# Performance work log

Hardware: AMD Instinct MI355X
Metric: run time of the kernel (lower is better)

The kernel has to match this reference:

```python
import jax, jax.numpy as jnp
import numpy as np

SIZE_IMG = 512
STRIDE = 32
N_ANCHOR = 9
BOUND_AC_LO, BOUND_AC_HI = -0.2, 1.2
EPS = 1e-05
IOU_SCALE = 10000
NEG_TH_ACGT = int(IOU_SCALE * 0.3)
POS_TH_ACGT = int(IOU_SCALE * 0.5)
POS_TH_GTAC = int(IOU_SCALE * 0.01)
NUM_POS_RPN = 128
NUM_NEG_RPN = 128
B, N_GT = 512, 32


def _anchors_rel(size_img, stride):
    h_fm = w_fm = size_img // stride
    # scales: closest floor power of 2 of min image side
    smax = 2 ** (size_img).bit_length()
    scales = np.array([smax >> 3, smax >> 2, smax >> 1], dtype=np.float32)
    sqrt2 = 1.4142135624
    ratio_hw = np.array([[sqrt2, sqrt2 / 2], [1, 1], [sqrt2 / 2, sqrt2]], dtype=np.float32)
    # (9,2) heights/widths: 3 scales x 3 ratios
    hw = (scales[:, None, None] * ratio_hw[None]).reshape(9, 2)
    ys = (np.arange(h_fm, dtype=np.float32) * stride + stride // 2)
    xs = (np.arange(w_fm, dtype=np.float32) * stride + stride // 2)
    cy = np.tile(ys[:, None, None], (1, w_fm, N_ANCHOR))
    cx = np.tile(xs[None, :, None], (h_fm, 1, N_ANCHOR))
    ctr = np.stack([cy, cx], axis=-1)                      # (H,W,9,2)
    hw_half = 0.5 * np.tile(hw[None, None], (h_fm, w_fm, 1, 1))
    ac_abs = np.concatenate([ctr - hw_half, ctr + hw_half], axis=-1).reshape(-1, 4)
    ac = ac_abs / np.float32(size_img)                     # relative (ymin,xmin,ymax,xmax)
    keep = ((ac[:, 0] >= BOUND_AC_LO) & (ac[:, 1] >= BOUND_AC_LO)
            & (ac[:, 2] <= BOUND_AC_HI) & (ac[:, 3] <= BOUND_AC_HI)
            & (ac[:, 2] > ac[:, 0]) & (ac[:, 3] > ac[:, 1]))
    return ac[keep].astype(np.float32)                     # (1384, 4)


def setup_inputs() -> dict:
    key = jax.random.key(0)
    k1, k2, k3, k4 = jax.random.split(key, 4)
    # valid GT boxes: sorted coord pairs in [0,1]
    yy = jnp.sort(jax.random.uniform(k1, (B, N_GT, 2)), axis=-1)
    xx = jnp.sort(jax.random.uniform(k2, (B, N_GT, 2)), axis=-1)
    bx_gt = jnp.stack([yy[..., 0], xx[..., 0], yy[..., 1], xx[..., 1]], axis=-1)
    ac_val = jnp.asarray(_anchors_rel(SIZE_IMG, STRIDE))
    rand_pos = jax.random.uniform(k3, (B, ac_val.shape[0]))
    rand_neg = jax.random.uniform(k4, (B, ac_val.shape[0]))
    return {"bx_gt": bx_gt, "ac_val": ac_val, "rand_pos": rand_pos, "rand_neg": rand_neg}


def _iou_mat(ac, gt):
    # ac (N_ac,4), gt (B,N_gt,4) -> (B,N_ac,N_gt)
    a = ac[None, :, None, :]
    g = gt[:, None, :, :]
    ih = jnp.clip(jnp.minimum(a[..., 2], g[..., 2]) - jnp.maximum(a[..., 0], g[..., 0]), 0.0)
    iw = jnp.clip(jnp.minimum(a[..., 3], g[..., 3]) - jnp.maximum(a[..., 1], g[..., 1]), 0.0)
    inter = ih * iw
    area_ac = (ac[:, 2] - ac[:, 0]) * (ac[:, 3] - ac[:, 1])
    area_gt = (gt[..., 2] - gt[..., 0]) * (gt[..., 3] - gt[..., 1])
    union = area_ac[None, :, None] + area_gt[:, None, :] - inter
    return inter / (union + EPS)


def _bbox2delta(bx_l, bx_r):
    h_r = jnp.maximum(bx_r[..., 2] - bx_r[..., 0], EPS)
    w_r = jnp.maximum(bx_r[..., 3] - bx_r[..., 1], EPS)
    yc_r = bx_r[..., 0] + 0.5 * (bx_r[..., 2] - bx_r[..., 0])
    xc_r = bx_r[..., 1] + 0.5 * (bx_r[..., 3] - bx_r[..., 1])
    h_l = bx_l[..., 2] - bx_l[..., 0]
    w_l = bx_l[..., 3] - bx_l[..., 1]
    yc_l = bx_l[..., 0] + 0.5 * h_l
    xc_l = bx_l[..., 1] + 0.5 * w_l
    d = jnp.stack([(xc_l - xc_r) / w_r, (yc_l - yc_r) / h_r,
                   jnp.log(w_l / w_r), jnp.log(h_l / h_r)], axis=-1)
    return jnp.clip(d, -10.0, 10.0)


def _sample_mask(mask, num, rand):
    th = num / (jnp.sum(mask, axis=-1, keepdims=True) + 1e-06)
    return jnp.where(rand < th, 1.0, 0.0) * mask


def reference(bx_gt, ac_val, rand_pos, rand_neg):
    iou = _iou_mat(ac_val, bx_gt)                          # (B, N_ac, N_gt)
    ious = (iou * IOU_SCALE).astype(jnp.int32)             # scale-integer IoU
    best_gt = jnp.argmax(ious, axis=-1)                    # (B, N_ac)
    iou_acgt = jnp.max(ious, axis=-1)                      # (B, N_ac)
    best_ac = jnp.argmax(ious, axis=1)                     # (B, N_gt)
    iou_gtac = jnp.max(ious, axis=1)                       # (B, N_gt)
    b, n_ac = iou_acgt.shape
    valid_gtac = (iou_gtac >= POS_TH_GTAC).astype(jnp.float32)
    pos_gtac = jnp.zeros((b, n_ac), jnp.float32).at[
        jnp.arange(b)[:, None], best_ac].max(valid_gtac) > 0.5
    pos = (iou_acgt >= POS_TH_ACGT) | pos_gtac             # (B, N_ac)
    neg = (iou_acgt < NEG_TH_ACGT) & (~pos)
    gt_match = bx_gt[jnp.arange(b)[:, None], best_gt]      # (B, N_ac, 4)
    bx_tgt = jnp.where(pos[..., None], gt_match,
                       jnp.where(neg[..., None], -2.0, -1.0))
    coor_sum = jnp.sum(bx_tgt, axis=-1)
    mask_fg = jnp.where(coor_sum > -4.0, 1.0, 0.0)
    mask_bg = jnp.where(coor_sum <= -8.0, 1.0, 0.0)
    mask_pos = _sample_mask(mask_fg, NUM_POS_RPN, rand_pos)
    mask_neg = _sample_mask(mask_bg, NUM_NEG_RPN, rand_neg)
    ac_b = jnp.broadcast_to(ac_val[None], bx_tgt.shape)
    bx_safe = jnp.where(pos[..., None], bx_tgt, ac_b)      # avoid log of negatives
    bx_del = _bbox2delta(bx_safe, ac_b)
    return jnp.concatenate(
        [bx_tgt, bx_del, mask_pos[..., None], mask_neg[..., None]], axis=-1)
```

## Files before the change

kernel.cpp:

```cpp
#include <hip/hip_runtime.h>

#define NGT   32
#define EPSF  1e-5f
#define GTAC_BIT (1 << 20)
#define APT   3
#define K1SPAN (APT * 256)

__global__ __launch_bounds__(256) void rpn_k1(
    const float* __restrict__ bx_gt,
    const float* __restrict__ ac_val,
    int* __restrict__ pack,
    int* __restrict__ colkey,
    int* __restrict__ partial,
    int n_ac)
{
    #pragma clang fp contract(off)
    const int b = blockIdx.y, chunk = blockIdx.x, tid = threadIdx.x;
    const int w = tid >> 6, lane = tid & 63;

    __shared__ int s_wk[NGT * 4];
    __shared__ int s_c[8];

    const float4* __restrict__ gtp = (const float4*)(bx_gt + (size_t)b * NGT * 4);

    int ckey[NGT];
    #pragma unroll
    for (int g = 0; g < NGT; ++g) ckey[g] = 0;

    int cf = 0, cb = 0;

    for (int j = 0; j < APT; ++j) {
        const int a = chunk * K1SPAN + j * 256 + tid;
        const bool active = (a < n_ac);
        float a0 = 0.f, a1 = 0.f, a2 = 0.f, a3 = 0.f;
        if (active) {
            float4 av = ((const float4*)ac_val)[a];
            a0 = av.x; a1 = av.y; a2 = av.z; a3 = av.w;
        }
        const float area = (a2 - a0) * (a3 - a1);

        int rkey = -1;
        const int akey = active ? (4095 - a) : -1;
        #pragma unroll
        for (int g = 0; g < NGT; ++g) {
            const float4 g4 = gtp[g];
            const float area_g = (g4.z - g4.x) * (g4.w - g4.y);
            float ih = fmaxf(fminf(a2, g4.z) - fmaxf(a0, g4.x), 0.0f);
            float iw = fmaxf(fminf(a3, g4.w) - fmaxf(a1, g4.y), 0.0f);
            float inter = ih * iw;
            float uni = area + area_g - inter;
            float iou = inter / (uni + EPSF);
            int v = (int)(iou * 10000.0f);
            int rk = (v << 5) | (31 - g);
            rkey = max(rkey, rk);
            int key = active ? ((v << 12) | (4095 - a)) : 0;
            ckey[g] = max(ckey[g], key);
        }
        if (active) {
            pack[(size_t)b * n_ac + a] = rkey;
            const int vmax = rkey >> 5;
            cf += (vmax >= 5000);
            cb += (vmax < 3000);
        }
    }

    #pragma unroll
    for (int g = 0; g < NGT; ++g) {
        int k = ckey[g];
        #pragma unroll
        for (int off = 32; off >= 1; off >>= 1)
            k = max(k, __shfl_xor(k, off, 64));
        if (lane == 0) s_wk[g*4 + w] = k;
    }

    #pragma unroll
    for (int off = 32; off >= 1; off >>= 1) {
        cf += __shfl_xor(cf, off, 64);
        cb += __shfl_xor(cb, off, 64);
    }
    if (lane == 0) { s_c[w*2] = cf; s_c[w*2+1] = cb; }
    __syncthreads();

    if (tid < NGT) {
        int k = max(max(s_wk[tid*4+0], s_wk[tid*4+1]),
                    max(s_wk[tid*4+2], s_wk[tid*4+3]));
        atomicMax(&colkey[b * NGT + tid], k);
    }
    if (tid == 0) {
        partial[(b * gridDim.x + chunk) * 2 + 0] = s_c[0] + s_c[2] + s_c[4] + s_c[6];
        partial[(b * gridDim.x + chunk) * 2 + 1] = s_c[1] + s_c[3] + s_c[5] + s_c[7];
    }
}

__global__ __launch_bounds__(64) void rpn_k2(
    int* __restrict__ pack,
    const int* __restrict__ colkey,
    const int* __restrict__ partial,
    float* __restrict__ th,
    int n_ac, int n_chunk)
{
    const int b = blockIdx.x, tid = threadIdx.x;

    int pf = 0, pb = 0;
    if (tid < n_chunk) {
        pf = partial[(b * n_chunk + tid) * 2 + 0];
        pb = partial[(b * n_chunk + tid) * 2 + 1];
    }
    #pragma unroll
    for (int off = 32; off >= 1; off >>= 1) {
        pf += __shfl_xor(pf, off, 64);
        pb += __shfl_xor(pb, off, 64);
    }

    int valid = 0, a = 0;
    if (tid < NGT) {
        int key = colkey[b * NGT + tid];
        int v = key >> 12;
        a = 4095 - (key & 4095);
        valid = (v >= 100);
    }
    int av = valid ? a : (0x10000 + tid);
    bool dup = false;
    for (int gp = 0; gp < NGT; ++gp) {
        int o = __shfl(av, gp, 64);
        if (gp < tid && o == av) dup = true;
    }
    bool contrib = valid && !dup;
    int rm = 0x7FFF;
    if (contrib) rm = pack[(size_t)b * n_ac + a] >> 5;
    unsigned long long m1 = __ballot(contrib && rm < 5000);
    unsigned long long m2 = __ballot(contrib && rm < 3000);

    if (contrib) atomicOr(&pack[(size_t)b * n_ac + a], GTAC_BIT);

    if (tid == 0) {
        int cf = pf + __popcll(m1);
        int cb = pb - __popcll(m2);
        th[b*2 + 0] = 128.0f / ((float)cf + 1e-6f);
        th[b*2 + 1] = 128.0f / ((float)cb + 1e-6f);
    }
}

__global__ __launch_bounds__(256) void rpn_k3(
    const float* __restrict__ bx_gt,
    const float* __restrict__ ac_val,
    const float* __restrict__ rand_pos,
    const float* __restrict__ rand_neg,
    const int* __restrict__ pack,
    const float* __restrict__ th,
    float* __restrict__ out,
    int n_ac)
{
    #pragma clang fp contract(off)
    const int b = blockIdx.y, chunk = blockIdx.x, tid = threadIdx.x;

    __shared__ float s_gt[NGT * 4];
    __shared__ float s_o[10 * 257];

    if (tid < NGT * 4) s_gt[tid] = bx_gt[(size_t)b * NGT * 4 + tid];
    __syncthreads();

    const int a = chunk * 256 + tid;
    if (a < n_ac) {
        const float th_pos = th[b*2 + 0];
        const float th_neg = th[b*2 + 1];
        const int p = pack[(size_t)b * n_ac + a];
        const bool gtac = (p & GTAC_BIT) != 0;
        const int rm = (p >> 5) & 0x7FFF;
        const int bg = 31 - (p & 31);
        const bool pos = (rm >= 5000) || gtac;
        const bool neg = !pos && (rm < 3000);

        const float4 avv = ((const float4*)ac_val)[a];
        const float a0 = avv.x, a1 = avv.y, a2 = avv.z, a3 = avv.w;

        float o0, o1, o2, o3, o4, o5, o6, o7;
        if (pos) {
            float g0 = s_gt[bg*4+0], g1 = s_gt[bg*4+1];
            float g2 = s_gt[bg*4+2], g3 = s_gt[bg*4+3];
            o0 = g0; o1 = g1; o2 = g2; o3 = g3;
            float hr = fmaxf(a2 - a0, EPSF);
            float wr = fmaxf(a3 - a1, EPSF);
            float ycr = a0 + 0.5f * (a2 - a0);
            float xcr = a1 + 0.5f * (a3 - a1);
            float hl = g2 - g0, wl = g3 - g1;
            float ycl = g0 + 0.5f * hl;
            float xcl = g1 + 0.5f * wl;
            o4 = fminf(fmaxf((xcl - xcr) / wr, -10.0f), 10.0f);
            o5 = fminf(fmaxf((ycl - ycr) / hr, -10.0f), 10.0f);
            o6 = fminf(fmaxf(logf(wl / wr), -10.0f), 10.0f);
            o7 = fminf(fmaxf(logf(hl / hr), -10.0f), 10.0f);
        } else {
            float t = neg ? -2.0f : -1.0f;
            o0 = o1 = o2 = o3 = t;
            o4 = o5 = o6 = o7 = 0.0f;
        }
        const float o8 = (pos && rand_pos[(size_t)b * n_ac + a] < th_pos) ? 1.0f : 0.0f;
        const float o9 = (neg && rand_neg[(size_t)b * n_ac + a] < th_neg) ? 1.0f : 0.0f;

        s_o[0*257 + tid] = o0; s_o[1*257 + tid] = o1;
        s_o[2*257 + tid] = o2; s_o[3*257 + tid] = o3;
        s_o[4*257 + tid] = o4; s_o[5*257 + tid] = o5;
        s_o[6*257 + tid] = o6; s_o[7*257 + tid] = o7;
        s_o[8*257 + tid] = o8; s_o[9*257 + tid] = o9;
    }
    __syncthreads();

    const int na_blk = min(256, n_ac - chunk * 256);
    const int nd = na_blk * 10;
    float* dst = out + ((size_t)b * n_ac + (size_t)chunk * 256) * 10;
    #pragma unroll
    for (int m = 0; m < 10; ++m) {
        const int idx = m * 256 + tid;
        if (idx < nd) {
            const int al = idx / 10, k = idx - al * 10;
            dst[idx] = s_o[k * 257 + al];
        }
    }
}

extern "C" void kernel_launch(void* const* d_in, const int* in_sizes, int n_in,
                              void* d_out, int out_size, void* d_ws, size_t ws_size,
                              hipStream_t stream) {
    const float* bx_gt    = (const float*)d_in[0];
    const float* ac_val   = (const float*)d_in[1];
    const float* rand_pos = (const float*)d_in[2];
    const float* rand_neg = (const float*)d_in[3];
    float* out = (float*)d_out;

    const int n_ac     = in_sizes[1] / 4;
    const int B        = in_sizes[2] / n_ac;
    const int n_chunk1 = (n_ac + K1SPAN - 1) / K1SPAN;
    const int n_chunk3 = (n_ac + 255) / 256;

    int* pack    = (int*)d_ws;
    int* colkey  = pack + (size_t)B * n_ac;
    int* partial = colkey + (size_t)B * NGT;
    float* th    = (float*)(partial + (size_t)B * n_chunk1 * 2);

    rpn_k1<<<dim3(n_chunk1, B), 256, 0, stream>>>(bx_gt, ac_val, pack, colkey, partial, n_ac);
    rpn_k2<<<B, 64, 0, stream>>>(pack, colkey, partial, th, n_ac, n_chunk1);
    rpn_k3<<<dim3(n_chunk3, B), 256, 0, stream>>>(bx_gt, ac_val, rand_pos, rand_neg,
                                                  pack, th, out, n_ac);
}
```

Baseline: 114.3 us.

## Fuse three RPN kernels into one per-batch block with shared-memory state

Merges the IoU/argmax kernel, the GT-to-anchor fixup kernel and the output kernel into a single kernel with one 256-thread block per image. The per-anchor pack array, column keys, counts and thresholds stay in LDS instead of global workspace. This removes two kernel launches, the global atomics and the workspace round-trips. In exchange the grid drops to B blocks, each looping over all anchors serially, so there is less parallelism per image. It also adds a MAXA limit of 2048 anchors.

```diff
diff --git a/kernel.cpp b/kernel.cpp
--- a/kernel.cpp
+++ b/kernel.cpp
@@ -1,46 +1,43 @@
 #include <hip/hip_runtime.h>
 
 #define NGT   32
+#define MAXA  2048
 #define EPSF  1e-5f
 #define GTAC_BIT (1 << 20)
-#define APT   3
-#define K1SPAN (APT * 256)
 
-__global__ __launch_bounds__(256) void rpn_k1(
+__global__ __launch_bounds__(256) void rpn_fused(
     const float* __restrict__ bx_gt,
     const float* __restrict__ ac_val,
-    int* __restrict__ pack,
-    int* __restrict__ colkey,
-    int* __restrict__ partial,
+    const float* __restrict__ rand_pos,
+    const float* __restrict__ rand_neg,
+    float* __restrict__ out,
     int n_ac)
 {
     #pragma clang fp contract(off)
-    const int b = blockIdx.y, chunk = blockIdx.x, tid = threadIdx.x;
+    const int b = blockIdx.x, tid = threadIdx.x;
     const int w = tid >> 6, lane = tid & 63;
 
-    __shared__ int s_wk[NGT * 4];
-    __shared__ int s_c[8];
+    __shared__ int   s_pack[MAXA];
+    __shared__ int   s_wk[NGT * 4];
+    __shared__ int   s_c[8];
+    __shared__ float s_th[2];
+    __shared__ float s_gt[NGT * 4];
+    __shared__ float s_o[10 * 257];
+
+    if (tid < NGT * 4) s_gt[tid] = bx_gt[(size_t)b * NGT * 4 + tid];
 
     const float4* __restrict__ gtp = (const float4*)(bx_gt + (size_t)b * NGT * 4);
 
     int ckey[NGT];
     #pragma unroll
     for (int g = 0; g < NGT; ++g) ckey[g] = 0;
-
     int cf = 0, cb = 0;
 
-    for (int j = 0; j < APT; ++j) {
-        const int a = chunk * K1SPAN + j * 256 + tid;
-        const bool active = (a < n_ac);
-        float a0 = 0.f, a1 = 0.f, a2 = 0.f, a3 = 0.f;
-        if (active) {
-            float4 av = ((const float4*)ac_val)[a];
-            a0 = av.x; a1 = av.y; a2 = av.z; a3 = av.w;
-        }
+    for (int a = tid; a < n_ac; a += 256) {
+        const float4 av = ((const float4*)ac_val)[a];
+        const float a0 = av.x, a1 = av.y, a2 = av.z, a3 = av.w;
         const float area = (a2 - a0) * (a3 - a1);
-
         int rkey = -1;
-        const int akey = active ? (4095 - a) : -1;
         #pragma unroll
         for (int g = 0; g < NGT; ++g) {
             const float4 g4 = gtp[g];
@@ -51,17 +48,13 @@
             float uni = area + area_g - inter;
             float iou = inter / (uni + EPSF);
             int v = (int)(iou * 10000.0f);
-            int rk = (v << 5) | (31 - g);
-            rkey = max(rkey, rk);
-            int key = active ? ((v << 12) | (4095 - a)) : 0;
-            ckey[g] = max(ckey[g], key);
+            rkey = max(rkey, (v << 5) | (31 - g));
+            ckey[g] = max(ckey[g], (v << 12) | (4095 - a));
         }
-        if (active) {
-            pack[(size_t)b * n_ac + a] = rkey;
-            const int vmax = rkey >> 5;
-            cf += (vmax >= 5000);
-            cb += (vmax < 3000);
-        }
+        s_pack[a] = rkey;
+        const int vmax = rkey >> 5;
+        cf += (vmax >= 5000);
+        cb += (vmax < 3000);
     }
 
     #pragma unroll
@@ -72,7 +65,6 @@
             k = max(k, __shfl_xor(k, off, 64));
         if (lane == 0) s_wk[g*4 + w] = k;
     }
-
     #pragma unroll
     for (int off = 32; off >= 1; off >>= 1) {
         cf += __shfl_xor(cf, off, 64);
@@ -81,141 +73,96 @@
     if (lane == 0) { s_c[w*2] = cf; s_c[w*2+1] = cb; }
     __syncthreads();
 
-    if (tid < NGT) {
-        int k = max(max(s_wk[tid*4+0], s_wk[tid*4+1]),
-                    max(s_wk[tid*4+2], s_wk[tid*4+3]));
-        atomicMax(&colkey[b * NGT + tid], k);
-    }
-    if (tid == 0) {
-        partial[(b * gridDim.x + chunk) * 2 + 0] = s_c[0] + s_c[2] + s_c[4] + s_c[6];
-        partial[(b * gridDim.x + chunk) * 2 + 1] = s_c[1] + s_c[3] + s_c[5] + s_c[7];
-    }
-}
-
-__global__ __launch_bounds__(64) void rpn_k2(
-    int* __restrict__ pack,
-    const int* __restrict__ colkey,
-    const int* __restrict__ partial,
-    float* __restrict__ th,
-    int n_ac, int n_chunk)
-{
-    const int b = blockIdx.x, tid = threadIdx.x;
-
-    int pf = 0, pb = 0;
-    if (tid < n_chunk) {
-        pf = partial[(b * n_chunk + tid) * 2 + 0];
-        pb = partial[(b * n_chunk + tid) * 2 + 1];
-    }
-    #pragma unroll
-    for (int off = 32; off >= 1; off >>= 1) {
-        pf += __shfl_xor(pf, off, 64);
-        pb += __shfl_xor(pb, off, 64);
-    }
-
-    int valid = 0, a = 0;
-    if (tid < NGT) {
-        int key = colkey[b * NGT + tid];
-        int v = key >> 12;
-        a = 4095 - (key & 4095);
-        valid = (v >= 100);
-    }
-    int av = valid ? a : (0x10000 + tid);
-    bool dup = false;
-    for (int gp = 0; gp < NGT; ++gp) {
-        int o = __shfl(av, gp, 64);
-        if (gp < tid && o == av) dup = true;
-    }
-    bool contrib = valid && !dup;
-    int rm = 0x7FFF;
-    if (contrib) rm = pack[(size_t)b * n_ac + a] >> 5;
-    unsigned long long m1 = __ballot(contrib && rm < 5000);
-    unsigned long long m2 = __ballot(contrib && rm < 3000);
-
-    if (contrib) atomicOr(&pack[(size_t)b * n_ac + a], GTAC_BIT);
-
-    if (tid == 0) {
-        int cf = pf + __popcll(m1);
-        int cb = pb - __popcll(m2);
-        th[b*2 + 0] = 128.0f / ((float)cf + 1e-6f);
-        th[b*2 + 1] = 128.0f / ((float)cb + 1e-6f);
-    }
-}
-
-__global__ __launch_bounds__(256) void rpn_k3(
-    const float* __restrict__ bx_gt,
-    const float* __restrict__ ac_val,
-    const float* __restrict__ rand_pos,
-    const float* __restrict__ rand_neg,
-    const int* __restrict__ pack,
-    const float* __restrict__ th,
-    float* __restrict__ out,
-    int n_ac)
-{
-    #pragma clang fp contract(off)
-    const int b = blockIdx.y, chunk = blockIdx.x, tid = threadIdx.x;
-
-    __shared__ float s_gt[NGT * 4];
-    __shared__ float s_o[10 * 257];
-
-    if (tid < NGT * 4) s_gt[tid] = bx_gt[(size_t)b * NGT * 4 + tid];
-    __syncthreads();
-
-    const int a = chunk * 256 + tid;
-    if (a < n_ac) {
-        const float th_pos = th[b*2 + 0];
-        const float th_neg = th[b*2 + 1];
-        const int p = pack[(size_t)b * n_ac + a];
-        const bool gtac = (p & GTAC_BIT) != 0;
-        const int rm = (p >> 5) & 0x7FFF;
-        const int bg = 31 - (p & 31);
-        const bool pos = (rm >= 5000) || gtac;
-        const bool neg = !pos && (rm < 3000);
-
-        const float4 avv = ((const float4*)ac_val)[a];
-        const float a0 = avv.x, a1 = avv.y, a2 = avv.z, a3 = avv.w;
-
-        float o0, o1, o2, o3, o4, o5, o6, o7;
-        if (pos) {
-            float g0 = s_gt[bg*4+0], g1 = s_gt[bg*4+1];
-            float g2 = s_gt[bg*4+2], g3 = s_gt[bg*4+3];
-            o0 = g0; o1 = g1; o2 = g2; o3 = g3;
-            float hr = fmaxf(a2 - a0, EPSF);
-            float wr = fmaxf(a3 - a1, EPSF);
-            float ycr = a0 + 0.5f * (a2 - a0);
-            float xcr = a1 + 0.5f * (a3 - a1);
-            float hl = g2 - g0, wl = g3 - g1;
-            float ycl = g0 + 0.5f * hl;
-            float xcl = g1 + 0.5f * wl;
-            o4 = fminf(fmaxf((xcl - xcr) / wr, -10.0f), 10.0f);
-            o5 = fminf(fmaxf((ycl - ycr) / hr, -10.0f), 10.0f);
-            o6 = fminf(fmaxf(logf(wl / wr), -10.0f), 10.0f);
-            o7 = fminf(fmaxf(logf(hl / hr), -10.0f), 10.0f);
-        } else {
-            float t = neg ? -2.0f : -1.0f;
-            o0 = o1 = o2 = o3 = t;
-            o4 = o5 = o6 = o7 = 0.0f;
+    if (w == 0) {
+        int valid = 0, a = 0;
+        if (lane < NGT) {
+            int key = max(max(s_wk[lane*4+0], s_wk[lane*4+1]),
+                          max(s_wk[lane*4+2], s_wk[lane*4+3]));
+            int v = key >> 12;
+            a = 4095 - (key & 4095);
+            valid = (v >= 100);
         }
-        const float o8 = (pos && rand_pos[(size_t)b * n_ac + a] < th_pos) ? 1.0f : 0.0f;
-        const float o9 = (neg && rand_neg[(size_t)b * n_ac + a] < th_neg) ? 1.0f : 0.0f;
-
-        s_o[0*257 + tid] = o0; s_o[1*257 + tid] = o1;
-        s_o[2*257 + tid] = o2; s_o[3*257 + tid] = o3;
-        s_o[4*257 + tid] = o4; s_o[5*257 + tid] = o5;
-        s_o[6*257 + tid] = o6; s_o[7*257 + tid] = o7;
-        s_o[8*257 + tid] = o8; s_o[9*257 + tid] = o9;
+        int avs = valid ? a : (0x10000 + lane);
+        bool dup = false;
+        #pragma unroll
+        for (int gp = 0; gp < NGT; ++gp) {
+            int o = __shfl(avs, gp, 64);
+            if (gp < lane && o == avs) dup = true;
+        }
+        const bool contrib = valid && !dup;
+        int rm = 0x7FFF;
+        if (contrib) rm = s_pack[a] >> 5;
+        unsigned long long m1 = __ballot(contrib && rm < 5000);
+        unsigned long long m2 = __ballot(contrib && rm < 3000);
+        if (contrib) atomicOr(&s_pack[a], GTAC_BIT);
+        if (lane == 0) {
+            int cff = s_c[0]+s_c[2]+s_c[4]+s_c[6] + __popcll(m1);
+            int cbb = s_c[1]+s_c[3]+s_c[5]+s_c[7] - __popcll(m2);
+            s_th[0] = 128.0f / ((float)cff + 1e-6f);
+            s_th[1] = 128.0f / ((float)cbb + 1e-6f);
+        }
     }
     __syncthreads();
 
-    const int na_blk = min(256, n_ac - chunk * 256);
-    const int nd = na_blk * 10;
-    float* dst = out + ((size_t)b * n_ac + (size_t)chunk * 256) * 10;
-    #pragma unroll
-    for (int m = 0; m < 10; ++m) {
-        const int idx = m * 256 + tid;
-        if (idx < nd) {
-            const int al = idx / 10, k = idx - al * 10;
-            dst[idx] = s_o[k * 257 + al];
+    const float th_pos = s_th[0], th_neg = s_th[1];
+    const int nround = (n_ac + 255) >> 8;
+    for (int r = 0; r < nround; ++r) {
+        const int a = r * 256 + tid;
+        if (a < n_ac) {
+            const int p = s_pack[a];
+            const bool gtac = (p & GTAC_BIT) != 0;
+            const int rm = (p >> 5) & 0x7FFF;
+            const int bg = 31 - (p & 31);
+            const bool pos = (rm >= 5000) || gtac;
+            const bool neg = !pos && (rm < 3000);
+
+            const float4 avv = ((const float4*)ac_val)[a];
+            const float a0 = avv.x, a1 = avv.y, a2 = avv.z, a3 = avv.w;
+
+            float o0, o1, o2, o3, o4, o5, o6, o7;
+            if (pos) {
+                float g0 = s_gt[bg*4+0], g1 = s_gt[bg*4+1];
+                float g2 = s_gt[bg*4+2], g3 = s_gt[bg*4+3];
+                o0 = g0; o1 = g1; o2 = g2; o3 = g3;
+                float hr = fmaxf(a2 - a0, EPSF);
+                float wr = fmaxf(a3 - a1, EPSF);
+                float ycr = a0 + 0.5f * (a2 - a0);
+                float xcr = a1 + 0.5f * (a3 - a1);
+                float hl = g2 - g0, wl = g3 - g1;
+                float ycl = g0 + 0.5f * hl;
+                float xcl = g1 + 0.5f * wl;
+                o4 = fminf(fmaxf((xcl - xcr) / wr, -10.0f), 10.0f);
+                o5 = fminf(fmaxf((ycl - ycr) / hr, -10.0f), 10.0f);
+                o6 = fminf(fmaxf(logf(wl / wr), -10.0f), 10.0f);
+                o7 = fminf(fmaxf(logf(hl / hr), -10.0f), 10.0f);
+            } else {
+                float t = neg ? -2.0f : -1.0f;
+                o0 = o1 = o2 = o3 = t;
+                o4 = o5 = o6 = o7 = 0.0f;
+            }
+            const float o8 = (pos && rand_pos[(size_t)b * n_ac + a] < th_pos) ? 1.0f : 0.0f;
+            const float o9 = (neg && rand_neg[(size_t)b * n_ac + a] < th_neg) ? 1.0f : 0.0f;
+
+            s_o[0*257 + tid] = o0; s_o[1*257 + tid] = o1;
+            s_o[2*257 + tid] = o2; s_o[3*257 + tid] = o3;
+            s_o[4*257 + tid] = o4; s_o[5*257 + tid] = o5;
+            s_o[6*257 + tid] = o6; s_o[7*257 + tid] = o7;
+            s_o[8*257 + tid] = o8; s_o[9*257 + tid] = o9;
         }
+        __syncthreads();
+
+        const int na_blk = min(256, n_ac - r * 256);
+        const int nd = na_blk * 10;
+        float* dst = out + ((size_t)b * n_ac + (size_t)r * 256) * 10;
+        #pragma unroll
+        for (int m = 0; m < 10; ++m) {
+            const int idx = m * 256 + tid;
+            if (idx < nd) {
+                const int al = idx / 10, k = idx - al * 10;
+                dst[idx] = s_o[k * 257 + al];
+            }
+        }
+        __syncthreads();
     }
 }
 
@@ -228,18 +175,8 @@
     const float* rand_neg = (const float*)d_in[3];
     float* out = (float*)d_out;
 
-    const int n_ac     = in_sizes[1] / 4;
-    const int B        = in_sizes[2] / n_ac;
-    const int n_chunk1 = (n_ac + K1SPAN - 1) / K1SPAN;
-    const int n_chunk3 = (n_ac + 255) / 256;
+    const int n_ac = in_sizes[1] / 4;
+    const int B    = in_sizes[2] / n_ac;
 
-    int* pack    = (int*)d_ws;
-    int* colkey  = pack + (size_t)B * n_ac;
-    int* partial = colkey + (size_t)B * NGT;
-    float* th    = (float*)(partial + (size_t)B * n_chunk1 * 2);
-
-    rpn_k1<<<dim3(n_chunk1, B), 256, 0, stream>>>(bx_gt, ac_val, pack, colkey, partial, n_ac);
-    rpn_k2<<<B, 64, 0, stream>>>(pack, colkey, partial, th, n_ac, n_chunk1);
-    rpn_k3<<<dim3(n_chunk3, B), 256, 0, stream>>>(bx_gt, ac_val, rand_pos, rand_neg,
-                                                  pack, th, out, n_ac);
+    rpn_fused<<<B, 256, 0, stream>>>(bx_gt, ac_val, rand_pos, rand_neg, out, n_ac);
 }
```

After: 126.8 us. +11.0%, slower.
